# Optimization experiments

Measured on AMD Instinct MI355X. Metric: run time of the kernel, lower is better.

Reference implementation:

```python
import jax, jax.numpy as jnp
import numpy as np

QMIN, QMAX = -128.0, 127.0


def setup_inputs() -> dict:
    key = jax.random.key(0)
    k1, k2, k3 = jax.random.split(key, 3)
    x = jax.random.normal(k1, (8, 32, 32, 32), jnp.float32)          # NCHW
    weight = jax.random.normal(k2, (32, 32, 3, 3), jnp.float32) * 0.1  # OIHW
    bias = jax.random.normal(k3, (32,), jnp.float32) * 0.01
    # lut[i, j] = (i - 128) * (j - 128), indexed by (q + 128).
    i = jnp.arange(256, dtype=jnp.float32) - 128.0
    lut = i[:, None] * i[None, :]
    return {"x": x, "weight": weight, "bias": bias, "lut": lut}


def reference(x, weight, bias, lut):
    # dynamic per-tensor scales (qmethod = ('dynamic','tensor','tensor'))
    sf = jax.lax.stop_gradient(jnp.max(jnp.abs(x)) / 127.0)
    sw = jax.lax.stop_gradient(jnp.max(jnp.abs(weight)) / 127.0)

    qx = jnp.clip(jnp.round(x / sf), QMIN, QMAX)        # int8 values as float
    qw = jnp.clip(jnp.round(weight / sw), QMIN, QMAX)

    # STE fake-quant tensors (forward = dequant, backward = identity)
    x_fq = x + jax.lax.stop_gradient(qx * sf - x)
    w_fq = weight + jax.lax.stop_gradient(qw * sw - weight)

    pad = ((1, 1), (1, 1))
    conv_fq = jax.lax.conv_general_dilated(
        x_fq, w_fq, window_strides=(1, 1), padding=pad,
        dimension_numbers=('NCHW', 'OIHW', 'NCHW'))

    # ---- LUT-based int8 conv path (forward value) ----
    # im2col on the int8 activation codes; zero padding -> q=0 -> index 128,
    # and lut[128, :] == 0, matching zero-padded conv.
    patches = jax.lax.conv_general_dilated_patches(
        qx, filter_shape=(3, 3), window_strides=(1, 1), padding=pad)
    N, K, Hp, Wp = patches.shape                       # K = Cin*kh*kw
    O = qw.shape[0]
    ix = (patches + 128.0).astype(jnp.int32).reshape(N, K, Hp * Wp)
    ix = jnp.transpose(ix, (0, 2, 1))                  # [N, P, K]
    iw = (qw.reshape(O, K) + 128.0).astype(jnp.int32)  # [O, K]

    # gather approximate products and accumulate over the window
    prods = lut[ix[:, :, None, :], iw[None, None, :, :]]  # [N, P, O, K]
    out_lut = (sf * sw) * jnp.sum(prods, axis=-1)          # [N, P, O]
    out_lut = jnp.transpose(out_lut, (0, 2, 1)).reshape(N, O, Hp, Wp)

    b = bias[None, :, None, None]
    out_fq = conv_fq + b
    out_lut = out_lut + b
    # forward returns the LUT result; gradients flow through the fake-quant conv (STE)
    return out_fq + jax.lax.stop_gradient(out_lut - out_fq)
```

## Files before the change

kernel.cpp:

```cpp
#include <hip/hip_runtime.h>

#define X_N 262144
#define W_N 9216
#define QX_PER_N (34*34*32)
#define QX_BYTES (8*QX_PER_N)
#define QX_INT4 (QX_BYTES/16)

static __device__ __forceinline__ int dot4(int a, int b, int acc) {
#if defined(__has_builtin)
#if __has_builtin(__builtin_amdgcn_sdot4)
  return __builtin_amdgcn_sdot4(a, b, acc, false);
#define DOT4_DONE 1
#endif
#endif
#ifndef DOT4_DONE
  #pragma unroll
  for (int k = 0; k < 4; k++)
    acc += ((a >> (8*k)) << 24 >> 24) * ((b >> (8*k)) << 24 >> 24);
  return acc;
#endif
}

__global__ __launch_bounds__(256) void k_partial_max(
    const float4* __restrict__ x4, const float4* __restrict__ w4,
    float* __restrict__ partials, int4* __restrict__ qx_zero) {
  int b = blockIdx.x, t = threadIdx.x;
  if (b >= 66) {
    for (int i = (b - 66) * 256 + t; i < QX_INT4; i += 8 * 256)
      qx_zero[i] = make_int4(0, 0, 0, 0);
    return;
  }
  __shared__ float red[256];
  float m = 0.f;
  if (b < 64) {
    #pragma unroll
    for (int k = 0; k < 4; k++) {
      float4 v = x4[b * 1024 + k * 256 + t];
      m = fmaxf(m, fmaxf(fmaxf(fabsf(v.x), fabsf(v.y)), fmaxf(fabsf(v.z), fabsf(v.w))));
    }
  } else {
    for (int i = (b - 64) * 256 + t; i < W_N / 4; i += 2 * 256) {
      float4 v = w4[i];
      m = fmaxf(m, fmaxf(fmaxf(fabsf(v.x), fabsf(v.y)), fmaxf(fabsf(v.z), fabsf(v.w))));
    }
  }
  red[t] = m;
  __syncthreads();
  #pragma unroll
  for (int s = 128; s >= 1; s >>= 1) {
    if (t < s) red[t] = fmaxf(red[t], red[t + s]);
    __syncthreads();
  }
  if (t == 0) partials[b] = red[0];
}

__global__ __launch_bounds__(256) void k_finalize_qw(
    const float* __restrict__ w, const float* __restrict__ partials,
    float* __restrict__ sfsw, signed char* __restrict__ qw_r) {
  __shared__ float red[64];
  __shared__ float s_sw;
  int t = threadIdx.x;
  if (t < 64) red[t] = partials[t];
  __syncthreads();
  if (t < 32) red[t] = fmaxf(red[t], red[t + 32]);
  __syncthreads();
  if (t < 16) red[t] = fmaxf(red[t], red[t + 16]);
  __syncthreads();
  if (t < 8) red[t] = fmaxf(red[t], red[t + 8]);
  __syncthreads();
  if (t == 0) {
    float mx = red[0];
    for (int i = 1; i < 8; i++) mx = fmaxf(mx, red[i]);
    float mw = fmaxf(partials[64], partials[65]);
    float sf = mx / 127.f;
    float sw = mw / 127.f;
    sfsw[0] = sf;
    sfsw[1] = sw;
    s_sw = sw;
  }
  __syncthreads();
  float sw = s_sw;
  for (int i = t; i < W_N; i += 256) {
    int o = i / 288, rem = i % 288;
    int c = rem / 9, k9 = rem % 9;
    float r = rintf(w[i] / sw);
    r = fminf(fmaxf(r, -128.f), 127.f);
    qw_r[(o * 9 + k9) * 32 + c] = (signed char)(int)r;
  }
}

__global__ __launch_bounds__(256) void k_quant_x(
    const float* __restrict__ x, const float* __restrict__ sfsw,
    signed char* __restrict__ qx) {
  int p = blockIdx.x * 256 + threadIdx.x;
  int n = p >> 10, hw = p & 1023;
  int h = hw >> 5, w = hw & 31;
  float inv_sf = 1.f / sfsw[0];
  int q[8];
  #pragma unroll
  for (int g = 0; g < 8; g++) {
    int packed = 0;
    #pragma unroll
    for (int j = 0; j < 4; j++) {
      int c = g * 4 + j;
      float v = x[n * 32768 + c * 1024 + hw];
      float r = fminf(fmaxf(rintf(v * inv_sf), -128.f), 127.f);
      packed |= ((int)r & 0xff) << (8 * j);
    }
    q[g] = packed;
  }
  int4* dst = (int4*)(qx + n * QX_PER_N + ((h + 1) * 34 + (w + 1)) * 32);
  dst[0] = make_int4(q[0], q[1], q[2], q[3]);
  dst[1] = make_int4(q[4], q[5], q[6], q[7]);
}

__global__ __launch_bounds__(256) void k_conv(
    const signed char* __restrict__ qx, const signed char* __restrict__ qw_r,
    const float* __restrict__ bias, const float* __restrict__ sfsw,
    float* __restrict__ out) {
  int b = blockIdx.x;
  int strip = b & 3;
  int o = (b >> 2) & 31;
  int n = b >> 7;
  int t = threadIdx.x;
  int h = strip * 8 + (t >> 5);
  int w = t & 31;

  const signed char* qxn = qx + n * QX_PER_N;
  const int* wq = (const int*)qw_r + o * 72;

  int acc = 0;
  #pragma unroll
  for (int ky = 0; ky < 3; ky++) {
    const int4* row = (const int4*)(qxn + ((h + ky) * 34 + w) * 32);
    int4 p0 = row[0], p1 = row[1], p2 = row[2], p3 = row[3], p4 = row[4], p5 = row[5];
    const int* wr = wq + ky * 24;
    acc = dot4(p0.x, wr[0],  acc); acc = dot4(p0.y, wr[1],  acc);
    acc = dot4(p0.z, wr[2],  acc); acc = dot4(p0.w, wr[3],  acc);
    acc = dot4(p1.x, wr[4],  acc); acc = dot4(p1.y, wr[5],  acc);
    acc = dot4(p1.z, wr[6],  acc); acc = dot4(p1.w, wr[7],  acc);
    acc = dot4(p2.x, wr[8],  acc); acc = dot4(p2.y, wr[9],  acc);
    acc = dot4(p2.z, wr[10], acc); acc = dot4(p2.w, wr[11], acc);
    acc = dot4(p3.x, wr[12], acc); acc = dot4(p3.y, wr[13], acc);
    acc = dot4(p3.z, wr[14], acc); acc = dot4(p3.w, wr[15], acc);
    acc = dot4(p4.x, wr[16], acc); acc = dot4(p4.y, wr[17], acc);
    acc = dot4(p4.z, wr[18], acc); acc = dot4(p4.w, wr[19], acc);
    acc = dot4(p5.x, wr[20], acc); acc = dot4(p5.y, wr[21], acc);
    acc = dot4(p5.z, wr[22], acc); acc = dot4(p5.w, wr[23], acc);
  }

  float scale = sfsw[0] * sfsw[1];
  out[(n * 32 + o) * 1024 + h * 32 + w] = scale * (float)acc + bias[o];
}

extern "C" void kernel_launch(void* const* d_in, const int* in_sizes, int n_in,
                              void* d_out, int out_size, void* d_ws, size_t ws_size,
                              hipStream_t stream) {
  const float* x    = (const float*)d_in[0];
  const float* w    = (const float*)d_in[1];
  const float* bias = (const float*)d_in[2];
  float* out = (float*)d_out;

  char* ws = (char*)d_ws;
  float*       partials = (float*)(ws + 0);
  float*       sfsw     = (float*)(ws + 1024);
  signed char* qw_r     = (signed char*)(ws + 2048);
  signed char* qx       = (signed char*)(ws + 16384);

  k_partial_max<<<74, 256, 0, stream>>>((const float4*)x, (const float4*)w,
                                        partials, (int4*)qx);
  k_finalize_qw<<<1, 256, 0, stream>>>(w, partials, sfsw, qw_r);
  k_quant_x<<<32, 256, 0, stream>>>(x, sfsw, qx);
  k_conv<<<1024, 256, 0, stream>>>(qx, qw_r, bias, sfsw, out);
}
```

Before: 75.00 us.

## Fuse scale reduction, weight quant and activation quant into one cooperative kernel

Three pre-processing kernels (partial max plus zeroing, finalize plus weight quantization, activation quantization) are merged into a single kernel launched cooperatively on 256 blocks. A grid-wide sync separates the global max reduction from the quantization phase. Every block redundantly reduces the weight max, and the weight and activation quantization work is spread across all blocks. This removes two kernel launches and the serial single-block finalize step, at the cost of cooperative-launch overhead and a grid barrier.

```diff
diff --git a/kernel.cpp b/kernel.cpp
--- a/kernel.cpp
+++ b/kernel.cpp
@@ -1,6 +1,8 @@
 #include <hip/hip_runtime.h>
+#include <hip/hip_cooperative_groups.h>
 
-#define X_N 262144
+namespace cg = cooperative_groups;
+
 #define W_N 9216
 #define QX_PER_N (34*34*32)
 #define QX_BYTES (8*QX_PER_N)
@@ -21,30 +23,27 @@
 #endif
 }
 
-__global__ __launch_bounds__(256) void k_partial_max(
-    const float4* __restrict__ x4, const float4* __restrict__ w4,
-    float* __restrict__ partials, int4* __restrict__ qx_zero) {
+__global__ __launch_bounds__(256) void k_prep(
+    const float* __restrict__ x, const float* __restrict__ w,
+    float* __restrict__ partials, float* __restrict__ sfsw,
+    signed char* __restrict__ qw_r, signed char* __restrict__ qx) {
+  __shared__ float red[256];
   int b = blockIdx.x, t = threadIdx.x;
-  if (b >= 66) {
-    for (int i = (b - 66) * 256 + t; i < QX_INT4; i += 8 * 256)
-      qx_zero[i] = make_int4(0, 0, 0, 0);
-    return;
+  int gid = b * 256 + t;
+
+  float4 v = ((const float4*)x)[gid];
+  float mx = fmaxf(fmaxf(fabsf(v.x), fabsf(v.y)), fmaxf(fabsf(v.z), fabsf(v.w)));
+
+  float mw = 0.f;
+  #pragma unroll
+  for (int i = t; i < W_N / 4; i += 256) {
+    float4 u = ((const float4*)w)[i];
+    mw = fmaxf(mw, fmaxf(fmaxf(fabsf(u.x), fabsf(u.y)), fmaxf(fabsf(u.z), fabsf(u.w))));
   }
-  __shared__ float red[256];
-  float m = 0.f;
-  if (b < 64) {
-    #pragma unroll
-    for (int k = 0; k < 4; k++) {
-      float4 v = x4[b * 1024 + k * 256 + t];
-      m = fmaxf(m, fmaxf(fmaxf(fabsf(v.x), fabsf(v.y)), fmaxf(fabsf(v.z), fabsf(v.w))));
-    }
-  } else {
-    for (int i = (b - 64) * 256 + t; i < W_N / 4; i += 2 * 256) {
-      float4 v = w4[i];
-      m = fmaxf(m, fmaxf(fmaxf(fabsf(v.x), fabsf(v.y)), fmaxf(fabsf(v.z), fabsf(v.w))));
-    }
-  }
-  red[t] = m;
+
+  if (gid < QX_INT4) ((int4*)qx)[gid] = make_int4(0, 0, 0, 0);
+
+  red[t] = mx;
   __syncthreads();
   #pragma unroll
   for (int s = 128; s >= 1; s >>= 1) {
@@ -52,66 +51,59 @@
     __syncthreads();
   }
   if (t == 0) partials[b] = red[0];
-}
+  red[t] = mw;
+  __syncthreads();
+  #pragma unroll
+  for (int s = 128; s >= 1; s >>= 1) {
+    if (t < s) red[t] = fmaxf(red[t], red[t + s]);
+    __syncthreads();
+  }
+  float sw = red[0] / 127.f;
 
-__global__ __launch_bounds__(256) void k_finalize_qw(
-    const float* __restrict__ w, const float* __restrict__ partials,
-    float* __restrict__ sfsw, signed char* __restrict__ qw_r) {
-  __shared__ float red[64];
-  __shared__ float s_sw;
-  int t = threadIdx.x;
-  if (t < 64) red[t] = partials[t];
+  cg::this_grid().sync();
+
+  red[t] = partials[t];
   __syncthreads();
-  if (t < 32) red[t] = fmaxf(red[t], red[t + 32]);
-  __syncthreads();
-  if (t < 16) red[t] = fmaxf(red[t], red[t + 16]);
-  __syncthreads();
-  if (t < 8) red[t] = fmaxf(red[t], red[t + 8]);
-  __syncthreads();
-  if (t == 0) {
-    float mx = red[0];
-    for (int i = 1; i < 8; i++) mx = fmaxf(mx, red[i]);
-    float mw = fmaxf(partials[64], partials[65]);
-    float sf = mx / 127.f;
-    float sw = mw / 127.f;
-    sfsw[0] = sf;
-    sfsw[1] = sw;
-    s_sw = sw;
+  #pragma unroll
+  for (int s = 128; s >= 1; s >>= 1) {
+    if (t < s) red[t] = fmaxf(red[t], red[t + s]);
+    __syncthreads();
   }
-  __syncthreads();
-  float sw = s_sw;
-  for (int i = t; i < W_N; i += 256) {
+  float sf = red[0] / 127.f;
+  float inv_sf = 1.f / sf;
+
+  if (gid == 0) { sfsw[0] = sf; sfsw[1] = sw; }
+
+  if (t >= 32 && t < 68) {
+    int i = b * 36 + (t - 32);
     int o = i / 288, rem = i % 288;
     int c = rem / 9, k9 = rem % 9;
     float r = rintf(w[i] / sw);
     r = fminf(fmaxf(r, -128.f), 127.f);
     qw_r[(o * 9 + k9) * 32 + c] = (signed char)(int)r;
   }
-}
 
-__global__ __launch_bounds__(256) void k_quant_x(
-    const float* __restrict__ x, const float* __restrict__ sfsw,
-    signed char* __restrict__ qx) {
-  int p = blockIdx.x * 256 + threadIdx.x;
-  int n = p >> 10, hw = p & 1023;
-  int h = hw >> 5, w = hw & 31;
-  float inv_sf = 1.f / sfsw[0];
-  int q[8];
-  #pragma unroll
-  for (int g = 0; g < 8; g++) {
-    int packed = 0;
+  if (t < 32) {
+    int p = b * 32 + t;
+    int n = p >> 10, hw = p & 1023;
+    int h = hw >> 5, ww = hw & 31;
+    int q[8];
     #pragma unroll
-    for (int j = 0; j < 4; j++) {
-      int c = g * 4 + j;
-      float v = x[n * 32768 + c * 1024 + hw];
-      float r = fminf(fmaxf(rintf(v * inv_sf), -128.f), 127.f);
-      packed |= ((int)r & 0xff) << (8 * j);
+    for (int g = 0; g < 8; g++) {
+      int packed = 0;
+      #pragma unroll
+      for (int j = 0; j < 4; j++) {
+        int c = g * 4 + j;
+        float vv = x[n * 32768 + c * 1024 + hw];
+        float rr = fminf(fmaxf(rintf(vv * inv_sf), -128.f), 127.f);
+        packed |= ((int)rr & 0xff) << (8 * j);
+      }
+      q[g] = packed;
     }
-    q[g] = packed;
+    int4* dst = (int4*)(qx + n * QX_PER_N + ((h + 1) * 34 + (ww + 1)) * 32);
+    dst[0] = make_int4(q[0], q[1], q[2], q[3]);
+    dst[1] = make_int4(q[4], q[5], q[6], q[7]);
   }
-  int4* dst = (int4*)(qx + n * QX_PER_N + ((h + 1) * 34 + (w + 1)) * 32);
-  dst[0] = make_int4(q[0], q[1], q[2], q[3]);
-  dst[1] = make_int4(q[4], q[5], q[6], q[7]);
 }
 
 __global__ __launch_bounds__(256) void k_conv(
@@ -156,6 +148,7 @@
 extern "C" void kernel_launch(void* const* d_in, const int* in_sizes, int n_in,
                               void* d_out, int out_size, void* d_ws, size_t ws_size,
                               hipStream_t stream) {
+  (void)in_sizes; (void)n_in; (void)out_size; (void)ws_size;
   const float* x    = (const float*)d_in[0];
   const float* w    = (const float*)d_in[1];
   const float* bias = (const float*)d_in[2];
@@ -167,9 +160,9 @@
   signed char* qw_r     = (signed char*)(ws + 2048);
   signed char* qx       = (signed char*)(ws + 16384);
 
-  k_partial_max<<<74, 256, 0, stream>>>((const float4*)x, (const float4*)w,
-                                        partials, (int4*)qx);
-  k_finalize_qw<<<1, 256, 0, stream>>>(w, partials, sfsw, qw_r);
-  k_quant_x<<<32, 256, 0, stream>>>(x, sfsw, qx);
+  void* args[6] = { (void*)&x, (void*)&w, (void*)&partials,
+                    (void*)&sfsw, (void*)&qw_r, (void*)&qx };
+  hipLaunchCooperativeKernel((const void*)k_prep, dim3(256), dim3(256),
+                             args, 0, stream);
   k_conv<<<1024, 256, 0, stream>>>(qx, qw_r, bias, sfsw, out);
 }
```

New measurement: 101.7 us. 35.5% more time.

## Fuse scale finalization, x quantization and conv into one kernel with LDS tiles

Applied to the files above, without the earlier changes.

Collapses the four-kernel pipeline into two. The first kernel computes x partial maxima and, in one block, the weight absmax and quantized weights. The second kernel reduces the x partials per block, quantizes a padded 4-row input tile into shared memory, and computes 16 output channels for 2 rows per block, reusing the loaded activations across channels. This removes the global padded qx buffer, its zeroing pass and two launches. The cost is that every block redoes the small partial reduction and quantizes overlapping halo rows.

```diff
diff --git a/kernel.cpp b/kernel.cpp
--- a/kernel.cpp
+++ b/kernel.cpp
@@ -1,10 +1,6 @@
 #include <hip/hip_runtime.h>
 
-#define X_N 262144
 #define W_N 9216
-#define QX_PER_N (34*34*32)
-#define QX_BYTES (8*QX_PER_N)
-#define QX_INT4 (QX_BYTES/16)
 
 static __device__ __forceinline__ int dot4(int a, int b, int acc) {
 #if defined(__has_builtin)
@@ -21,28 +17,38 @@
 #endif
 }
 
-__global__ __launch_bounds__(256) void k_partial_max(
-    const float4* __restrict__ x4, const float4* __restrict__ w4,
-    float* __restrict__ partials, int4* __restrict__ qx_zero) {
+__global__ __launch_bounds__(256) void k_absmax_wq(
+    const float4* __restrict__ x4, const float* __restrict__ w,
+    float* __restrict__ partials, float* __restrict__ sfsw,
+    signed char* __restrict__ qw_r) {
+  __shared__ float red[256];
+  __shared__ float s_sw;
   int b = blockIdx.x, t = threadIdx.x;
-  if (b >= 66) {
-    for (int i = (b - 66) * 256 + t; i < QX_INT4; i += 8 * 256)
-      qx_zero[i] = make_int4(0, 0, 0, 0);
-    return;
-  }
-  __shared__ float red[256];
-  float m = 0.f;
+
   if (b < 64) {
+    float m = 0.f;
     #pragma unroll
     for (int k = 0; k < 4; k++) {
       float4 v = x4[b * 1024 + k * 256 + t];
       m = fmaxf(m, fmaxf(fmaxf(fabsf(v.x), fabsf(v.y)), fmaxf(fabsf(v.z), fabsf(v.w))));
     }
-  } else {
-    for (int i = (b - 64) * 256 + t; i < W_N / 4; i += 2 * 256) {
-      float4 v = w4[i];
-      m = fmaxf(m, fmaxf(fmaxf(fabsf(v.x), fabsf(v.y)), fmaxf(fabsf(v.z), fabsf(v.w))));
+    red[t] = m;
+    __syncthreads();
+    #pragma unroll
+    for (int s = 128; s >= 1; s >>= 1) {
+      if (t < s) red[t] = fmaxf(red[t], red[t + s]);
+      __syncthreads();
     }
+    if (t == 0) partials[b] = red[0];
+    return;
+  }
+
+  const float4* w4 = (const float4*)w;
+  float m = 0.f;
+  #pragma unroll
+  for (int j = 0; j < 9; j++) {
+    float4 v = w4[t + 256 * j];
+    m = fmaxf(m, fmaxf(fmaxf(fabsf(v.x), fabsf(v.y)), fmaxf(fabsf(v.z), fabsf(v.w))));
   }
   red[t] = m;
   __syncthreads();
@@ -51,36 +57,12 @@
     if (t < s) red[t] = fmaxf(red[t], red[t + s]);
     __syncthreads();
   }
-  if (t == 0) partials[b] = red[0];
-}
-
-__global__ __launch_bounds__(256) void k_finalize_qw(
-    const float* __restrict__ w, const float* __restrict__ partials,
-    float* __restrict__ sfsw, signed char* __restrict__ qw_r) {
-  __shared__ float red[64];
-  __shared__ float s_sw;
-  int t = threadIdx.x;
-  if (t < 64) red[t] = partials[t];
-  __syncthreads();
-  if (t < 32) red[t] = fmaxf(red[t], red[t + 32]);
-  __syncthreads();
-  if (t < 16) red[t] = fmaxf(red[t], red[t + 16]);
-  __syncthreads();
-  if (t < 8) red[t] = fmaxf(red[t], red[t + 8]);
-  __syncthreads();
-  if (t == 0) {
-    float mx = red[0];
-    for (int i = 1; i < 8; i++) mx = fmaxf(mx, red[i]);
-    float mw = fmaxf(partials[64], partials[65]);
-    float sf = mx / 127.f;
-    float sw = mw / 127.f;
-    sfsw[0] = sf;
-    sfsw[1] = sw;
-    s_sw = sw;
-  }
+  if (t == 0) { s_sw = red[0] / 127.f; sfsw[1] = s_sw; }
   __syncthreads();
   float sw = s_sw;
-  for (int i = t; i < W_N; i += 256) {
+  #pragma unroll
+  for (int j = 0; j < 36; j++) {
+    int i = t + 256 * j;
     int o = i / 288, rem = i % 288;
     int c = rem / 9, k9 = rem % 9;
     float r = rintf(w[i] / sw);
@@ -89,73 +71,102 @@
   }
 }
 
-__global__ __launch_bounds__(256) void k_quant_x(
-    const float* __restrict__ x, const float* __restrict__ sfsw,
-    signed char* __restrict__ qx) {
-  int p = blockIdx.x * 256 + threadIdx.x;
-  int n = p >> 10, hw = p & 1023;
-  int h = hw >> 5, w = hw & 31;
-  float inv_sf = 1.f / sfsw[0];
-  int q[8];
+__global__ __launch_bounds__(256) void k_fused(
+    const float* __restrict__ x, const float* __restrict__ partials,
+    const float* __restrict__ sfsw, const signed char* __restrict__ qw_r,
+    const float* __restrict__ bias, float* __restrict__ out) {
+  __shared__ float red[64];
+  __shared__ float s_sf;
+  __shared__ __align__(16) int qxt[4][34][8];
+
+  int b = blockIdx.x, t = threadIdx.x;
+  int n = b >> 5, hpair = (b >> 1) & 15, ohalf = b & 1;
+  int h0 = hpair * 2;
+
+  int w = t & 31, g = t >> 5;
+  float xv[4][4];
   #pragma unroll
-  for (int g = 0; g < 8; g++) {
+  for (int r = 0; r < 4; r++) {
+    int y = h0 - 1 + r;
+    bool valid = (y >= 0) && (y < 32);
+    #pragma unroll
+    for (int j = 0; j < 4; j++) {
+      int c = g * 4 + j;
+      xv[r][j] = valid ? x[n * 32768 + c * 1024 + y * 32 + w] : 0.f;
+    }
+  }
+
+  if (t < 64) red[t] = partials[t];
+  __syncthreads();
+  if (t < 32) red[t] = fmaxf(red[t], red[t + 32]);
+  __syncthreads();
+  if (t < 16) red[t] = fmaxf(red[t], red[t + 16]);
+  __syncthreads();
+  if (t < 8)  red[t] = fmaxf(red[t], red[t + 8]);
+  __syncthreads();
+  if (t < 4)  red[t] = fmaxf(red[t], red[t + 4]);
+  __syncthreads();
+  if (t < 2)  red[t] = fmaxf(red[t], red[t + 2]);
+  __syncthreads();
+  if (t == 0) s_sf = fmaxf(red[0], red[1]) / 127.f;
+  __syncthreads();
+  float inv_sf = 1.f / s_sf;
+
+  #pragma unroll
+  for (int r = 0; r < 4; r++) {
     int packed = 0;
     #pragma unroll
     for (int j = 0; j < 4; j++) {
-      int c = g * 4 + j;
-      float v = x[n * 32768 + c * 1024 + hw];
-      float r = fminf(fmaxf(rintf(v * inv_sf), -128.f), 127.f);
-      packed |= ((int)r & 0xff) << (8 * j);
+      float rr = fminf(fmaxf(rintf(xv[r][j] * inv_sf), -128.f), 127.f);
+      packed |= ((int)rr & 0xff) << (8 * j);
     }
-    q[g] = packed;
+    qxt[r][w + 1][g] = packed;
   }
-  int4* dst = (int4*)(qx + n * QX_PER_N + ((h + 1) * 34 + (w + 1)) * 32);
-  dst[0] = make_int4(q[0], q[1], q[2], q[3]);
-  dst[1] = make_int4(q[4], q[5], q[6], q[7]);
-}
+  if (t < 64) {
+    int r = t >> 4, col = ((t >> 3) & 1) * 33, g2 = t & 7;
+    qxt[r][col][g2] = 0;
+  }
+  __syncthreads();
 
-__global__ __launch_bounds__(256) void k_conv(
-    const signed char* __restrict__ qx, const signed char* __restrict__ qw_r,
-    const float* __restrict__ bias, const float* __restrict__ sfsw,
-    float* __restrict__ out) {
-  int b = blockIdx.x;
-  int strip = b & 3;
-  int o = (b >> 2) & 31;
-  int n = b >> 7;
-  int t = threadIdx.x;
-  int h = strip * 8 + (t >> 5);
-  int w = t & 31;
+  int wv = t >> 6, l = t & 63;
+  int hs = l >> 5, ww = l & 31;
+  int h = h0 + hs;
 
-  const signed char* qxn = qx + n * QX_PER_N;
-  const int* wq = (const int*)qw_r + o * 72;
-
-  int acc = 0;
+  int4 p[3][6];
   #pragma unroll
-  for (int ky = 0; ky < 3; ky++) {
-    const int4* row = (const int4*)(qxn + ((h + ky) * 34 + w) * 32);
-    int4 p0 = row[0], p1 = row[1], p2 = row[2], p3 = row[3], p4 = row[4], p5 = row[5];
-    const int* wr = wq + ky * 24;
-    acc = dot4(p0.x, wr[0],  acc); acc = dot4(p0.y, wr[1],  acc);
-    acc = dot4(p0.z, wr[2],  acc); acc = dot4(p0.w, wr[3],  acc);
-    acc = dot4(p1.x, wr[4],  acc); acc = dot4(p1.y, wr[5],  acc);
-    acc = dot4(p1.z, wr[6],  acc); acc = dot4(p1.w, wr[7],  acc);
-    acc = dot4(p2.x, wr[8],  acc); acc = dot4(p2.y, wr[9],  acc);
-    acc = dot4(p2.z, wr[10], acc); acc = dot4(p2.w, wr[11], acc);
-    acc = dot4(p3.x, wr[12], acc); acc = dot4(p3.y, wr[13], acc);
-    acc = dot4(p3.z, wr[14], acc); acc = dot4(p3.w, wr[15], acc);
-    acc = dot4(p4.x, wr[16], acc); acc = dot4(p4.y, wr[17], acc);
-    acc = dot4(p4.z, wr[18], acc); acc = dot4(p4.w, wr[19], acc);
-    acc = dot4(p5.x, wr[20], acc); acc = dot4(p5.y, wr[21], acc);
-    acc = dot4(p5.z, wr[22], acc); acc = dot4(p5.w, wr[23], acc);
+  for (int r = 0; r < 3; r++) {
+    const int4* row = (const int4*)(&qxt[hs + r][ww][0]);
+    #pragma unroll
+    for (int k = 0; k < 6; k++) p[r][k] = row[k];
   }
 
-  float scale = sfsw[0] * sfsw[1];
-  out[(n * 32 + o) * 1024 + h * 32 + w] = scale * (float)acc + bias[o];
+  float scale = s_sf * sfsw[1];
+
+  #pragma unroll
+  for (int j = 0; j < 4; j++) {
+    int o = __builtin_amdgcn_readfirstlane(ohalf * 16 + wv * 4 + j);
+    const int* wr = (const int*)qw_r + o * 72;
+    int acc = 0;
+    #pragma unroll
+    for (int ky = 0; ky < 3; ky++) {
+      const int* wk = wr + ky * 24;
+      #pragma unroll
+      for (int k = 0; k < 6; k++) {
+        int4 pp = p[ky][k];
+        acc = dot4(pp.x, wk[k * 4 + 0], acc);
+        acc = dot4(pp.y, wk[k * 4 + 1], acc);
+        acc = dot4(pp.z, wk[k * 4 + 2], acc);
+        acc = dot4(pp.w, wk[k * 4 + 3], acc);
+      }
+    }
+    out[(n * 32 + o) * 1024 + h * 32 + ww] = scale * (float)acc + bias[o];
+  }
 }
 
 extern "C" void kernel_launch(void* const* d_in, const int* in_sizes, int n_in,
                               void* d_out, int out_size, void* d_ws, size_t ws_size,
                               hipStream_t stream) {
+  (void)in_sizes; (void)n_in; (void)out_size; (void)ws_size;
   const float* x    = (const float*)d_in[0];
   const float* w    = (const float*)d_in[1];
   const float* bias = (const float*)d_in[2];
@@ -163,13 +174,9 @@
 
   char* ws = (char*)d_ws;
   float*       partials = (float*)(ws + 0);
-  float*       sfsw     = (float*)(ws + 1024);
+  float*       sfsw     = (float*)(ws + 512);
   signed char* qw_r     = (signed char*)(ws + 2048);
-  signed char* qx       = (signed char*)(ws + 16384);
 
-  k_partial_max<<<74, 256, 0, stream>>>((const float4*)x, (const float4*)w,
-                                        partials, (int4*)qx);
-  k_finalize_qw<<<1, 256, 0, stream>>>(w, partials, sfsw, qw_r);
-  k_quant_x<<<32, 256, 0, stream>>>(x, sfsw, qx);
-  k_conv<<<1024, 256, 0, stream>>>(qx, qw_r, bias, sfsw, out);
+  k_absmax_wq<<<65, 256, 0, stream>>>((const float4*)x, w, partials, sfsw, qw_r);
+  k_fused<<<256, 256, 0, stream>>>(x, partials, sfsw, qw_r, bias, out);
 }
```

Measured after the change: 69.27 us. -7.6%, faster.
